# Kernel optimization log

Measured on AMD Instinct MI355X. Metric: run time of the kernel, lower is better.

Reference implementation:

```python
import jax, jax.numpy as jnp
import numpy as np

B, H, W, N, C = 2, 56, 56, 2, 128
NUM_HEADS = 8
SPLIT = 7
IDX = 0  # 0 -> H_sp = H, W_sp = split_size (vertical stripes)


def setup_inputs() -> dict:
    key = jax.random.key(0)
    k1, k2, k3, k4 = jax.random.split(key, 4)
    query = jax.random.normal(k1, (B, H, W, N, C), jnp.float32)
    key_t = jax.random.normal(k2, (B, H, W, N, C), jnp.float32)
    value = jax.random.normal(k3, (B, H, W, N, C), jnp.float32)
    conv_w = jax.random.normal(k4, (C, 1, 3, 3), jnp.float32) * 0.1  # depthwise get_v weight
    return {"query": query, "key": key_t, "value": value, "conv_w": conv_w}


def _im2cswin(x, Hsp, Wsp, h):
    # [b, Hp, Wp, n, c] -> [(b i j), h, Hsp*Wsp*n, d]
    b, Hp, Wp, n, c = x.shape
    i, j = Hp // Hsp, Wp // Wsp
    d = c // h
    x = x.reshape(b, i, Hsp, j, Wsp, n, h, d)
    x = x.transpose(0, 1, 3, 6, 2, 4, 5, 7)  # b i j h Hsp Wsp n d
    return x.reshape(b * i * j, h, Hsp * Wsp * n, d)


def _window_mask(Hsp, Wsp, n):
    # block attention between same spatial position / different candidates (except diagonal)
    pos = jnp.repeat(jnp.arange(Hsp * Wsp), n)
    L = pos.shape[0]
    m = jnp.where(pos[:, None] == pos[None, :], -jnp.inf, 0.0).astype(jnp.float32)
    m = m.at[jnp.arange(L), jnp.arange(L)].set(0.0)
    return m


def reference(query, key, value, conv_w):
    b, Hh, Ww, n, c = query.shape
    if IDX == -1:
        Hsp, Wsp = Hh, Ww
    elif IDX == 0:
        Hsp, Wsp = Hh, SPLIT
    else:
        Hsp, Wsp = SPLIT, Ww
    # H % Hsp == 0 and W % Wsp == 0 by construction -> no padding branch
    h = NUM_HEADS
    d = c // h
    scale = d ** (-0.5)

    q = _im2cswin(query, Hsp, Wsp, h)
    k = _im2cswin(key, Hsp, Wsp, h)
    v = _im2cswin(value, Hsp, Wsp, h)

    # rpe via depthwise 3x3 conv over the value (LePE-style), summed over candidates
    v_img = value.transpose(0, 3, 4, 1, 2).reshape(b * n, c, Hh, Ww)  # [b*n, C, H, W]
    conv = jax.lax.conv_general_dilated(
        v_img, conv_w, (1, 1), 'SAME',
        dimension_numbers=('NCHW', 'OIHW', 'NCHW'), feature_group_count=c)
    rpe = conv.reshape(b, n, c, Hh, Ww).sum(1, keepdims=True)
    center = conv_w[:, 0, 1, 1]  # center tap of each depthwise kernel
    self_scaled = (v_img * center[None, :, None, None]).reshape(b, n, c, Hh, Ww)
    self_scaled = self_scaled - self_scaled.sum(1, keepdims=True)
    rpe = (rpe + self_scaled).transpose(0, 3, 4, 1, 2)  # [b, H, W, n, c]

    mask = _window_mask(Hsp, Wsp, n)[None, None]  # [1,1,L,L]
    attn = jnp.einsum('bhid,bhjd->bhij', q * scale, k) + mask
    attn = jax.nn.softmax(attn.astype(jnp.float32), axis=-1).astype(q.dtype)
    x = jnp.einsum('bhij,bhjd->bhid', attn, v)

    # windows back to image layout
    i, j = Hh // Hsp, Ww // Wsp
    x = x.reshape(b, i, j, h, Hsp, Wsp, n, d)
    x = x.transpose(0, 1, 4, 2, 5, 6, 3, 7).reshape(b, Hh, Ww, n, c)
    return x + rpe
```

## Files before the change

kernel.cpp:

```cpp
#include <hip/hip_runtime.h>

typedef __bf16 bf16x8 __attribute__((ext_vector_type(8)));
typedef float f32x16 __attribute__((ext_vector_type(16)));
typedef unsigned u32x2 __attribute__((ext_vector_type(2)));

#define BB 2
#define HH 56
#define WW 56
#define NN 2
#define CC 128
#define NH 8
#define DD 16
#define WSP 7
#define LQ 784
#define KB_TOK 800
#define VT_STRIDE 808
#define NKC 25
#define NINST 128
#define BPI 5
#define NWAVE 5

#define K_OFF 0
#define V_OFF 25600
#define W_OFF 51456
#define ONES_OFF 52032
#define SMEM_BYTES 52064

#define QSCALE 0.3606737602222409f

union U2 { __bf16 h[2]; unsigned u; };
union U4 { unsigned u[4]; bf16x8 v; };
union H8 { bf16x8 v; uint4 q; };

static __device__ __forceinline__ float4 f4zero() { float4 r; r.x = r.y = r.z = r.w = 0.f; return r; }
static __device__ __forceinline__ float4 f4add(float4 a, float4 b) {
    float4 r; r.x = a.x + b.x; r.y = a.y + b.y; r.z = a.z + b.z; r.w = a.w + b.w; return r;
}
static __device__ __forceinline__ float4 f4fma(float4 acc, float4 w, float4 s) {
    acc.x += w.x * s.x; acc.y += w.y * s.y; acc.z += w.z * s.z; acc.w += w.w * s.w; return acc;
}

__global__ __launch_bounds__(320) void attn_fused(const float* __restrict__ q_g,
                                                  const float* __restrict__ k_g,
                                                  const float* __restrict__ v_g,
                                                  const float* __restrict__ conv_w,
                                                  float* __restrict__ out) {
    __shared__ alignas(16) char smem[SMEM_BYTES];
    __bf16* Klds = (__bf16*)(smem + K_OFF);
    __bf16* Vlds = (__bf16*)(smem + V_OFF);
    float*  wlds = (float*)(smem + W_OFF);
    __bf16* onesb = (__bf16*)(smem + ONES_OFF);

    const int bid  = blockIdx.x;
    const int g    = bid >> 3;
    const int inst = (bid & 7) + 8 * (g / BPI);
    const int part = g % BPI;
    const int head = inst & 7;
    const int win  = inst >> 3;
    const int b    = win >> 3, wj = win & 7;
    const int tid  = threadIdx.x;

    if (tid < 144) {
        int c = tid & 15, k = tid >> 4;
        wlds[k * 16 + c] = conv_w[(head * 16 + c) * 9 + k];
    } else if (tid < 160) {
        onesb[tid - 144] = (__bf16)1.f;
    }

    for (int tok = tid; tok < KB_TOK; tok += 320) {
        if (tok < LQ) {
            int pos = tok >> 1, n = tok & 1;
            int y = pos / WSP, xl2 = pos - y * WSP;
            long off = ((long)(((b * HH + y) * WW + wj * WSP + xl2) * NN + n)) * CC + head * DD;

            float kv[16], vv[16];
            *(float4*)&kv[0]  = *(const float4*)(k_g + off);
            *(float4*)&kv[4]  = *(const float4*)(k_g + off + 4);
            *(float4*)&kv[8]  = *(const float4*)(k_g + off + 8);
            *(float4*)&kv[12] = *(const float4*)(k_g + off + 12);
            *(float4*)&vv[0]  = *(const float4*)(v_g + off);
            *(float4*)&vv[4]  = *(const float4*)(v_g + off + 4);
            *(float4*)&vv[8]  = *(const float4*)(v_g + off + 8);
            *(float4*)&vv[12] = *(const float4*)(v_g + off + 12);

            H8 lo, hi;
#pragma unroll
            for (int i = 0; i < 8; ++i) { lo.v[i] = (__bf16)kv[i]; hi.v[i] = (__bf16)kv[8 + i]; }
            *(uint4*)&Klds[tok * 16]     = lo.q;
            *(uint4*)&Klds[tok * 16 + 8] = hi.q;
#pragma unroll
            for (int d = 0; d < 16; ++d)
                Vlds[d * VT_STRIDE + tok] = (__bf16)vv[d];
        } else {
            H8 z; z.q = make_uint4(0, 0, 0, 0);
            *(uint4*)&Klds[tok * 16]     = z.q;
            *(uint4*)&Klds[tok * 16 + 8] = z.q;
#pragma unroll
            for (int d = 0; d < 16; ++d)
                Vlds[d * VT_STRIDE + tok] = (__bf16)0.f;
        }
    }
    __syncthreads();

    const int w    = tid >> 6;
    const int lane = tid & 63;
    const int col  = lane & 31;
    const int h    = lane >> 5;
    const int qt   = part * NWAVE + w;
    const int myq  = qt * 32 + col;
    const int sib  = myq ^ 1;

    const int myqc = myq < LQ ? myq : LQ - 1;
    const int pos = myqc >> 1, n = myqc & 1;
    const int y = pos / WSP, xl = pos - y * WSP;
    const long ooff = ((long)(((b * HH + y) * WW + wj * WSP + xl) * NN + n)) * CC + head * DD;

    bf16x8 qfv;
    {
        const float* qp = q_g + ooff + 8 * h;
        float qv[8];
        *(float4*)&qv[0] = *(const float4*)qp;
        *(float4*)&qv[4] = *(const float4*)(qp + 4);
        H8 qq;
#pragma unroll
        for (int i = 0; i < 8; ++i) qq.v[i] = (__bf16)(qv[i] * QSCALE);
        qfv = qq.v;
    }

    f32x16 acc, zv;
#pragma unroll
    for (int i = 0; i < 16; ++i) { acc[i] = 0.f; zv[i] = 0.f; }

    const char* kbase = (const char*)Klds + col * 32 + h * 16;
    const char* vbase;
    int vstep, tstep;
    if (col < 16) {
        vbase = (const char*)Vlds + col * (VT_STRIDE * 2) + h * 16;
        vstep = 64; tstep = 32;
    } else {
        vbase = (const char*)onesb;
        vstep = 0; tstep = 0;
    }

    for (int c = 0; c < NKC; ++c) {
        bf16x8 kf = *(const bf16x8*)(kbase + c * 1024);

        f32x16 st = __builtin_amdgcn_mfma_f32_32x32x16_bf16(kf, qfv, zv, 0, 0, 0);

        float p[16];
        if (c == qt || c == NKC - 1) {
#pragma unroll
            for (int r = 0; r < 16; ++r) {
                int kr = (r & 3) + 8 * (r >> 2) + 4 * h;
                int gk = c * 32 + kr;
                p[r] = (gk >= LQ || gk == sib) ? 0.f : __builtin_amdgcn_exp2f(st[r]);
            }
        } else {
#pragma unroll
            for (int r = 0; r < 16; ++r) p[r] = __builtin_amdgcn_exp2f(st[r]);
        }

        unsigned pk[4][2];
#pragma unroll
        for (int b2 = 0; b2 < 4; ++b2) {
            U2 a, bb;
            a.h[0]  = (__bf16)p[4 * b2 + 0];
            a.h[1]  = (__bf16)p[4 * b2 + 1];
            bb.h[0] = (__bf16)p[4 * b2 + 2];
            bb.h[1] = (__bf16)p[4 * b2 + 3];
            pk[b2][0] = a.u;
            pk[b2][1] = bb.u;
        }

#pragma unroll
        for (int t = 0; t < 2; ++t) {
            U4 pb;
#pragma unroll
            for (int j = 0; j < 2; ++j) {
#if __has_builtin(__builtin_amdgcn_permlane32_swap)
                u32x2 rr = __builtin_amdgcn_permlane32_swap(pk[2 * t][j], pk[2 * t + 1][j], false, false);
                pb.u[j]     = rr[0];
                pb.u[2 + j] = rr[1];
#else
                unsigned swa = __shfl_xor(pk[2 * t][j], 32, 64);
                unsigned swb = __shfl_xor(pk[2 * t + 1][j], 32, 64);
                pb.u[j]     = h ? swb : pk[2 * t][j];
                pb.u[2 + j] = h ? pk[2 * t + 1][j] : swa;
#endif
            }
            bf16x8 vf = *(const bf16x8*)(vbase + c * vstep + t * tstep);
            acc = __builtin_amdgcn_mfma_f32_32x32x16_bf16(vf, pb.v, acc, 0, 0, 0);
        }
    }

    if (myq < LQ) {
        const int xg = wj * WSP + xl;
        const long rowbase = ((long)(b * HH + y) * WW + xg) * (NN * CC) + head * DD;

        float4 cv0 = f4zero(), cv1 = f4zero();
        float4 sc0 = f4zero(), sc1 = f4zero();
        float4 vn0 = f4zero(), vn1 = f4zero();

#pragma unroll
        for (int dy = -1; dy <= 1; ++dy) {
            int yy = y + dy;
#pragma unroll
            for (int dx = -1; dx <= 1; ++dx) {
                int xx = xg + dx;
                if (yy < 0 || yy >= HH || xx < 0 || xx >= WW) continue;
                int k = (dy + 1) * 3 + (dx + 1);
                const float* p = v_g + rowbase + ((long)dy * WW + dx) * (NN * CC);
                float4 a0 = *(const float4*)(p + 4 * h);
                float4 b0 = *(const float4*)(p + CC + 4 * h);
                float4 a1 = *(const float4*)(p + 8 + 4 * h);
                float4 b1 = *(const float4*)(p + CC + 8 + 4 * h);
                float4 w0 = *(const float4*)(wlds + k * 16 + 4 * h);
                float4 w1 = *(const float4*)(wlds + k * 16 + 8 + 4 * h);
                float4 S0 = f4add(a0, b0);
                float4 S1 = f4add(a1, b1);
                cv0 = f4fma(cv0, w0, S0);
                cv1 = f4fma(cv1, w1, S1);
                if (dy == 0 && dx == 0) {
                    sc0 = S0; sc1 = S1;
                    vn0 = n ? b0 : a0;
                    vn1 = n ? b1 : a1;
                }
            }
        }
        float4 wc0 = *(const float4*)(wlds + 4 * 16 + 4 * h);
        float4 wc1 = *(const float4*)(wlds + 4 * 16 + 8 + 4 * h);

        float inv = 1.f / acc[8];
        float* po = out + ooff;
        float4 r0, r1;
        r0.x = cv0.x + wc0.x * (vn0.x - sc0.x) + acc[0] * inv;
        r0.y = cv0.y + wc0.y * (vn0.y - sc0.y) + acc[1] * inv;
        r0.z = cv0.z + wc0.z * (vn0.z - sc0.z) + acc[2] * inv;
        r0.w = cv0.w + wc0.w * (vn0.w - sc0.w) + acc[3] * inv;
        r1.x = cv1.x + wc1.x * (vn1.x - sc1.x) + acc[4] * inv;
        r1.y = cv1.y + wc1.y * (vn1.y - sc1.y) + acc[5] * inv;
        r1.z = cv1.z + wc1.z * (vn1.z - sc1.z) + acc[6] * inv;
        r1.w = cv1.w + wc1.w * (vn1.w - sc1.w) + acc[7] * inv;
        *(float4*)(po + 4 * h) = r0;
        *(float4*)(po + 8 + 4 * h) = r1;
    }
}

extern "C" void kernel_launch(void* const* d_in, const int* in_sizes, int n_in,
                              void* d_out, int out_size, void* d_ws, size_t ws_size,
                              hipStream_t stream) {
    const float* q = (const float*)d_in[0];
    const float* k = (const float*)d_in[1];
    const float* v = (const float*)d_in[2];
    const float* w = (const float*)d_in[3];
    float* out = (float*)d_out;

    attn_fused<<<NINST * BPI, 320, 0, stream>>>(q, k, v, w, out);
}
```

Before: 37.71 us.

## Batch K/V global loads, swizzle K LDS layout, hoist Q load

Restructures the K/V staging loop so each thread issues all of its global loads for up to three tokens before any LDS writes, and hoists the Q load ahead of staging so global latency overlaps. K is stored in LDS with an XOR swizzle of its 16-byte chunks to reduce bank conflicts on the MFMA operand reads. The reciprocal of the row sum is also moved earlier. Holding three tokens of loaded data raises register pressure and may lower occupancy.

```diff
diff --git a/kernel.cpp b/kernel.cpp
--- a/kernel.cpp
+++ b/kernel.cpp
@@ -46,9 +46,9 @@
                                                   const float* __restrict__ conv_w,
                                                   float* __restrict__ out) {
     __shared__ alignas(16) char smem[SMEM_BYTES];
-    __bf16* Klds = (__bf16*)(smem + K_OFF);
-    __bf16* Vlds = (__bf16*)(smem + V_OFF);
-    float*  wlds = (float*)(smem + W_OFF);
+    uint4*  K16   = (uint4*)(smem + K_OFF);
+    __bf16* Vlds  = (__bf16*)(smem + V_OFF);
+    float*  wlds  = (float*)(smem + W_OFF);
     __bf16* onesb = (__bf16*)(smem + ONES_OFF);
 
     const int bid  = blockIdx.x;
@@ -60,48 +60,6 @@
     const int b    = win >> 3, wj = win & 7;
     const int tid  = threadIdx.x;
 
-    if (tid < 144) {
-        int c = tid & 15, k = tid >> 4;
-        wlds[k * 16 + c] = conv_w[(head * 16 + c) * 9 + k];
-    } else if (tid < 160) {
-        onesb[tid - 144] = (__bf16)1.f;
-    }
-
-    for (int tok = tid; tok < KB_TOK; tok += 320) {
-        if (tok < LQ) {
-            int pos = tok >> 1, n = tok & 1;
-            int y = pos / WSP, xl2 = pos - y * WSP;
-            long off = ((long)(((b * HH + y) * WW + wj * WSP + xl2) * NN + n)) * CC + head * DD;
-
-            float kv[16], vv[16];
-            *(float4*)&kv[0]  = *(const float4*)(k_g + off);
-            *(float4*)&kv[4]  = *(const float4*)(k_g + off + 4);
-            *(float4*)&kv[8]  = *(const float4*)(k_g + off + 8);
-            *(float4*)&kv[12] = *(const float4*)(k_g + off + 12);
-            *(float4*)&vv[0]  = *(const float4*)(v_g + off);
-            *(float4*)&vv[4]  = *(const float4*)(v_g + off + 4);
-            *(float4*)&vv[8]  = *(const float4*)(v_g + off + 8);
-            *(float4*)&vv[12] = *(const float4*)(v_g + off + 12);
-
-            H8 lo, hi;
-#pragma unroll
-            for (int i = 0; i < 8; ++i) { lo.v[i] = (__bf16)kv[i]; hi.v[i] = (__bf16)kv[8 + i]; }
-            *(uint4*)&Klds[tok * 16]     = lo.q;
-            *(uint4*)&Klds[tok * 16 + 8] = hi.q;
-#pragma unroll
-            for (int d = 0; d < 16; ++d)
-                Vlds[d * VT_STRIDE + tok] = (__bf16)vv[d];
-        } else {
-            H8 z; z.q = make_uint4(0, 0, 0, 0);
-            *(uint4*)&Klds[tok * 16]     = z.q;
-            *(uint4*)&Klds[tok * 16 + 8] = z.q;
-#pragma unroll
-            for (int d = 0; d < 16; ++d)
-                Vlds[d * VT_STRIDE + tok] = (__bf16)0.f;
-        }
-    }
-    __syncthreads();
-
     const int w    = tid >> 6;
     const int lane = tid & 63;
     const int col  = lane & 31;
@@ -115,15 +73,77 @@
     const int y = pos / WSP, xl = pos - y * WSP;
     const long ooff = ((long)(((b * HH + y) * WW + wj * WSP + xl) * NN + n)) * CC + head * DD;
 
+    float4 q0 = *(const float4*)(q_g + ooff + 8 * h);
+    float4 q1 = *(const float4*)(q_g + ooff + 8 * h + 4);
+
+    if (tid < 144) {
+        int c = tid & 15, k = tid >> 4;
+        wlds[k * 16 + c] = conv_w[(head * 16 + c) * 9 + k];
+    } else if (tid < 160) {
+        onesb[tid - 144] = (__bf16)1.f;
+    }
+
+    {
+        const int t0 = tid, t1 = tid + 320, t2 = tid + 640;
+        const bool v2 = t2 < KB_TOK;
+
+        auto tok_off = [&](int tok) -> long {
+            int tc = tok < LQ ? tok : LQ - 1;
+            int tpos = tc >> 1, tn = tc & 1;
+            int ty = tpos / WSP, txl = tpos - ty * WSP;
+            return ((long)(((b * HH + ty) * WW + wj * WSP + txl) * NN + tn)) * CC + head * DD;
+        };
+        const long o0 = tok_off(t0), o1 = tok_off(t1), o2 = v2 ? tok_off(t2) : o0;
+
+        float4 k00 = *(const float4*)(k_g + o0),      k01 = *(const float4*)(k_g + o0 + 4);
+        float4 k02 = *(const float4*)(k_g + o0 + 8),  k03 = *(const float4*)(k_g + o0 + 12);
+        float4 v00 = *(const float4*)(v_g + o0),      v01 = *(const float4*)(v_g + o0 + 4);
+        float4 v02 = *(const float4*)(v_g + o0 + 8),  v03 = *(const float4*)(v_g + o0 + 12);
+        float4 k10 = *(const float4*)(k_g + o1),      k11 = *(const float4*)(k_g + o1 + 4);
+        float4 k12 = *(const float4*)(k_g + o1 + 8),  k13 = *(const float4*)(k_g + o1 + 12);
+        float4 v10 = *(const float4*)(v_g + o1),      v11 = *(const float4*)(v_g + o1 + 4);
+        float4 v12 = *(const float4*)(v_g + o1 + 8),  v13 = *(const float4*)(v_g + o1 + 12);
+        float4 k20 = *(const float4*)(k_g + o2),      k21 = *(const float4*)(k_g + o2 + 4);
+        float4 k22 = *(const float4*)(k_g + o2 + 8),  k23 = *(const float4*)(k_g + o2 + 12);
+        float4 v20 = *(const float4*)(v_g + o2),      v21 = *(const float4*)(v_g + o2 + 4);
+        float4 v22 = *(const float4*)(v_g + o2 + 8),  v23 = *(const float4*)(v_g + o2 + 12);
+
+        auto wr = [&](int tok, bool valid, float4 ka, float4 kb, float4 kc, float4 kd,
+                      float4 va, float4 vb, float4 vc, float4 vd) {
+            float kv[16], vv[16];
+            *(float4*)&kv[0] = ka; *(float4*)&kv[4] = kb;
+            *(float4*)&kv[8] = kc; *(float4*)&kv[12] = kd;
+            *(float4*)&vv[0] = va; *(float4*)&vv[4] = vb;
+            *(float4*)&vv[8] = vc; *(float4*)&vv[12] = vd;
+            const bool live = valid && tok < LQ;
+            H8 lo, hi;
+#pragma unroll
+            for (int i = 0; i < 8; ++i) {
+                lo.v[i] = live ? (__bf16)kv[i]     : (__bf16)0.f;
+                hi.v[i] = live ? (__bf16)kv[8 + i] : (__bf16)0.f;
+            }
+            if (valid) {
+                int sw = tok & 7;
+                K16[(tok * 2)     ^ sw] = lo.q;
+                K16[(tok * 2 + 1) ^ sw] = hi.q;
+#pragma unroll
+                for (int d = 0; d < 16; ++d)
+                    Vlds[d * VT_STRIDE + tok] = live ? (__bf16)vv[d] : (__bf16)0.f;
+            }
+        };
+        wr(t0, true, k00, k01, k02, k03, v00, v01, v02, v03);
+        wr(t1, true, k10, k11, k12, k13, v10, v11, v12, v13);
+        wr(t2, v2,   k20, k21, k22, k23, v20, v21, v22, v23);
+    }
+    __syncthreads();
+
     bf16x8 qfv;
     {
-        const float* qp = q_g + ooff + 8 * h;
-        float qv[8];
-        *(float4*)&qv[0] = *(const float4*)qp;
-        *(float4*)&qv[4] = *(const float4*)(qp + 4);
         H8 qq;
-#pragma unroll
-        for (int i = 0; i < 8; ++i) qq.v[i] = (__bf16)(qv[i] * QSCALE);
+        qq.v[0] = (__bf16)(q0.x * QSCALE); qq.v[1] = (__bf16)(q0.y * QSCALE);
+        qq.v[2] = (__bf16)(q0.z * QSCALE); qq.v[3] = (__bf16)(q0.w * QSCALE);
+        qq.v[4] = (__bf16)(q1.x * QSCALE); qq.v[5] = (__bf16)(q1.y * QSCALE);
+        qq.v[6] = (__bf16)(q1.z * QSCALE); qq.v[7] = (__bf16)(q1.w * QSCALE);
         qfv = qq.v;
     }
 
@@ -131,7 +151,7 @@
 #pragma unroll
     for (int i = 0; i < 16; ++i) { acc[i] = 0.f; zv[i] = 0.f; }
 
-    const char* kbase = (const char*)Klds + col * 32 + h * 16;
+    const uint4* kbase = K16 + ((col * 2 + h) ^ (col & 7));
     const char* vbase;
     int vstep, tstep;
     if (col < 16) {
@@ -143,9 +163,9 @@
     }
 
     for (int c = 0; c < NKC; ++c) {
-        bf16x8 kf = *(const bf16x8*)(kbase + c * 1024);
-
-        f32x16 st = __builtin_amdgcn_mfma_f32_32x32x16_bf16(kf, qfv, zv, 0, 0, 0);
+        U4 kf;
+        *(uint4*)&kf = kbase[c * 64];
+        f32x16 st = __builtin_amdgcn_mfma_f32_32x32x16_bf16(kf.v, qfv, zv, 0, 0, 0);
 
         float p[16];
         if (c == qt || c == NKC - 1) {
@@ -194,6 +214,8 @@
     }
 
     if (myq < LQ) {
+        float inv = 1.f / acc[8];
+
         const int xg = wj * WSP + xl;
         const long rowbase = ((long)(b * HH + y) * WW + xg) * (NN * CC) + head * DD;
 
@@ -230,7 +252,6 @@
         float4 wc0 = *(const float4*)(wlds + 4 * 16 + 4 * h);
         float4 wc1 = *(const float4*)(wlds + 4 * 16 + 8 + 4 * h);
 
-        float inv = 1.f / acc[8];
         float* po = out + ooff;
         float4 r0, r1;
         r0.x = cv0.x + wc0.x * (vn0.x - sc0.x) + acc[0] * inv;
```

New measurement: 38.10 us. No clear change (+1.0%).
